# Kernel tuning notes

Measured on AMD Instinct MI355X. Metric: run time of the kernel, lower is better.

Reference implementation:

```python
import jax, jax.numpy as jnp
import numpy as np

N_HEAD = 16
HEAD_DIM = 32          # n_embed // n_head // 2
LAMBDA_INIT = 0.2      # 0.8 - 0.6*exp(-0.3*(layer-1)) with layer=1
ROPE_BASE = 10000.0
EPS = 1e-5


def _rope(x):
    # torchtune RotaryPositionalEmbeddings: interleaved adjacent pairs
    B, T, H, D = x.shape
    half = D // 2
    theta = ROPE_BASE ** (-(jnp.arange(half, dtype=jnp.float32) * 2.0 / D))  # [half]
    ang = jnp.arange(T, dtype=jnp.float32)[:, None] * theta[None, :]         # [T, half]
    cos = jnp.cos(ang)[None, :, None, :]
    sin = jnp.sin(ang)[None, :, None, :]
    xr = x.reshape(B, T, H, half, 2)
    x1, x2 = xr[..., 0], xr[..., 1]
    out = jnp.stack([x1 * cos - x2 * sin, x1 * sin + x2 * cos], axis=-1)
    return out.reshape(B, T, H, D).astype(x.dtype)


def reference(x, W_attn, W_proj, lambda_q1, lambda_k1, lambda_q2, lambda_k2):
    B, T, C = x.shape
    H, D = N_HEAD, HEAD_DIM
    qkv = x @ W_attn                              # [B,T,3C]
    q, k, v = jnp.split(qkv, 3, axis=-1)
    q = _rope(q.reshape(B, T, 2 * H, D)).transpose(0, 2, 1, 3)   # [B,2H,T,D]
    k = _rope(k.reshape(B, T, 2 * H, D)).transpose(0, 2, 1, 3)   # [B,2H,T,D]
    v = v.reshape(B, T, H, 2 * D).transpose(0, 2, 1, 3)          # [B,H,T,2D]

    lam = (jnp.exp(jnp.dot(lambda_q1, lambda_k1))
           - jnp.exp(jnp.dot(lambda_q2, lambda_k2)) + LAMBDA_INIT)

    # causal SDPA over both score paths (2H heads) in one pass, shared V
    scale = 1.0 / jnp.sqrt(jnp.asarray(D, x.dtype))
    scores = jnp.einsum('bhqd,bhkd->bhqk', q, k) * scale         # [B,2H,T,T]
    causal = jnp.tril(jnp.ones((T, T), dtype=bool))
    scores = jnp.where(causal, scores, jnp.finfo(scores.dtype).min)
    probs = jax.nn.softmax(scores, axis=-1)
    vv = jnp.concatenate([v, v], axis=1)                         # [B,2H,T,2D]
    A = jnp.einsum('bhqk,bhkd->bhqd', probs, vv)                 # [B,2H,T,2D]
    A1, A2 = A[:, :H], A[:, H:]

    diff = A1 - lam * A2                                         # [B,H,T,2D]
    # RMSNorm over last dim (2*head_dim), no affine, eps=1e-5
    diff = diff * jax.lax.rsqrt(jnp.mean(diff * diff, axis=-1, keepdims=True) + EPS)
    diff = (1.0 - LAMBDA_INIT) * diff
    out = diff.transpose(0, 2, 1, 3).reshape(B, T, C)
    return out @ W_proj


def setup_inputs() -> dict:
    key = jax.random.key(0)
    ks = jax.random.split(key, 7)
    B, T, C, D = 2, 2048, 1024, HEAD_DIM
    return {
        'x': jax.random.normal(ks[0], (B, T, C), jnp.float32),
        'W_attn': jax.random.normal(ks[1], (C, 3 * C), jnp.float32) * 0.02,
        'W_proj': jax.random.normal(ks[2], (C, C), jnp.float32) * 0.02,
        'lambda_q1': jax.random.normal(ks[3], (D,), jnp.float32) * 0.1,
        'lambda_k1': jax.random.normal(ks[4], (D,), jnp.float32) * 0.1,
        'lambda_q2': jax.random.normal(ks[5], (D,), jnp.float32) * 0.1,
        'lambda_k2': jax.random.normal(ks[6], (D,), jnp.float32) * 0.1,
    }
```

## Files before the change

### kernel.cpp

```cpp
#include <hip/hip_runtime.h>


typedef unsigned short u16;
typedef __bf16 bf16x8 __attribute__((ext_vector_type(8)));
typedef float f32x4 __attribute__((ext_vector_type(4)));
typedef float f32x16 __attribute__((ext_vector_type(16)));
typedef unsigned u32x2 __attribute__((ext_vector_type(2)));

__device__ __forceinline__ u16 f2bf(float f) {
  return __builtin_bit_cast(u16, (__bf16)f);
}
__device__ __forceinline__ float bf2f(u16 u) {
  return (float)__builtin_bit_cast(__bf16, u);
}
__device__ __forceinline__ unsigned pk2(float a, float b) {
  return (unsigned)f2bf(a) | ((unsigned)f2bf(b) << 16);
}

__device__ __forceinline__ void gload16(const u16* g, u16* l) {
  __builtin_amdgcn_global_load_lds(
      (const __attribute__((address_space(1))) unsigned int*)g,
      (__attribute__((address_space(3))) unsigned int*)l, 16, 0, 0);
}

__device__ __forceinline__ void trans_body(const float* __restrict__ in,
                                           u16* __restrict__ out, int R, int Cn,
                                           int bx, int by, float (*tile)[33],
                                           int tx, int ty) {
  const int c0 = bx * 32, r0 = by * 32;
#pragma unroll
  for (int rr = 0; rr < 4; ++rr)
    tile[ty + rr * 8][tx] = in[(size_t)(r0 + ty + rr * 8) * Cn + c0 + tx];
  __syncthreads();
#pragma unroll
  for (int rr = 0; rr < 4; ++rr)
    out[(size_t)(c0 + ty + rr * 8) * R + r0 + tx] = f2bf(tile[tx][ty + rr * 8]);
}

__global__ __launch_bounds__(256) void prep_kernel(
    const float* __restrict__ x, const float* __restrict__ Wa,
    const float* __restrict__ Wp, u16* __restrict__ xb, u16* __restrict__ WaT,
    u16* __restrict__ WpT) {
  __shared__ float tile[32][33];
  const int id = blockIdx.x;
  const int tx = threadIdx.x & 31, ty = threadIdx.x >> 5;
  if (id < 4096) {
    const int i = id * 256 + threadIdx.x;
    float4 v = ((const float4*)x)[i];
    ushort4 o;
    o.x = f2bf(v.x); o.y = f2bf(v.y); o.z = f2bf(v.z); o.w = f2bf(v.w);
    ((ushort4*)xb)[i] = o;
  } else if (id < 7168) {
    const int t = id - 4096;
    trans_body(Wa, WaT, 1024, 3072, t % 96, t / 96, tile, tx, ty);
  } else {
    const int t = id - 7168;
    trans_body(Wp, WpT, 1024, 1024, t & 31, t >> 5, tile, tx, ty);
  }
}

__global__ __launch_bounds__(256) void gemm_bf16_kernel(
    const u16* __restrict__ A, const u16* __restrict__ BT, u16* __restrict__ Cout,
    int Mdim, int Ndim, int Kdim) {
  __shared__ u16 As[128 * 32];
  __shared__ u16 Bs[128 * 32];
  const int tid = threadIdx.x;
  const int l = tid & 63;
  const int w = tid >> 6;
  const int nwgx = gridDim.x;
  const int lin = blockIdx.x + nwgx * blockIdx.y;
  const int cpx = (nwgx * gridDim.y) >> 3;
  const int swz = (lin & 7) * cpx + (lin >> 3);
  const int bm = swz / nwgx, bn = swz % nwgx;
  const int wm = w >> 1, wn = w & 1;
  const int rowA0 = bm * 128, rowB0 = bn * 128;
  const int r_ = tid >> 2;
  const int s_ = (tid & 3) * 8;
  const u16* Ag = &A[(size_t)(rowA0 + r_) * Kdim + s_];
  const u16* Bg = &BT[(size_t)(rowB0 + r_) * Kdim + s_];
  const size_t rstride = (size_t)64 * Kdim;
  f32x4 acc[4][4] = {};
  for (int k0 = 0; k0 < Kdim; k0 += 32) {
    gload16(Ag + k0, &As[r_ * 32 + s_]);
    gload16(Ag + rstride + k0, &As[2048 + r_ * 32 + s_]);
    gload16(Bg + k0, &Bs[r_ * 32 + s_]);
    gload16(Bg + rstride + k0, &Bs[2048 + r_ * 32 + s_]);
    __syncthreads();
    bf16x8 a[4], b[4];
#pragma unroll
    for (int i = 0; i < 4; ++i)
      a[i] = *(const bf16x8*)&As[(wm * 64 + i * 16 + (l & 15)) * 32 + (l >> 4) * 8];
#pragma unroll
    for (int j = 0; j < 4; ++j)
      b[j] = *(const bf16x8*)&Bs[(wn * 64 + j * 16 + (l & 15)) * 32 + (l >> 4) * 8];
#pragma unroll
    for (int i = 0; i < 4; ++i)
#pragma unroll
      for (int j = 0; j < 4; ++j)
        acc[i][j] = __builtin_amdgcn_mfma_f32_16x16x32_bf16(a[i], b[j], acc[i][j], 0, 0, 0);
    __syncthreads();
  }
  const int cr = (l >> 4) * 4;
  const int cc = l & 15;
#pragma unroll
  for (int i = 0; i < 4; ++i)
#pragma unroll
    for (int j = 0; j < 4; ++j)
#pragma unroll
      for (int r = 0; r < 4; ++r) {
        const int row = rowA0 + wm * 64 + i * 16 + cr + r;
        const int col = rowB0 + wn * 64 + j * 16 + cc;
        Cout[(size_t)row * Ndim + col] = f2bf(acc[i][j][r]);
      }
}

__global__ __launch_bounds__(256) void gemm_out_kernel(
    const u16* __restrict__ A, const u16* __restrict__ BT, float* __restrict__ Cout,
    int Mdim, int Ndim, int Kdim) {
  __shared__ u16 As[64 * 32];
  __shared__ u16 Bs[128 * 32];
  const int tid = threadIdx.x;
  const int l = tid & 63;
  const int w = tid >> 6;
  const int nwgx = gridDim.x;
  const int lin = blockIdx.x + nwgx * blockIdx.y;
  const int cpx = (nwgx * gridDim.y) >> 3;
  const int swz = (lin & 7) * cpx + (lin >> 3);
  const int bm = swz / nwgx, bn = swz % nwgx;
  const int wm = w >> 1, wn = w & 1;
  const int rowA0 = bm * 64, rowB0 = bn * 128;
  const int r_ = tid >> 2;
  const int s_ = (tid & 3) * 8;
  const u16* Ag = &A[(size_t)(rowA0 + r_) * Kdim + s_];
  const u16* Bg = &BT[(size_t)(rowB0 + r_) * Kdim + s_];
  const size_t rstride = (size_t)64 * Kdim;
  f32x4 acc[2][4] = {};
  for (int k0 = 0; k0 < Kdim; k0 += 32) {
    gload16(Ag + k0, &As[r_ * 32 + s_]);
    gload16(Bg + k0, &Bs[r_ * 32 + s_]);
    gload16(Bg + rstride + k0, &Bs[2048 + r_ * 32 + s_]);
    __syncthreads();
    bf16x8 a[2], b[4];
#pragma unroll
    for (int i = 0; i < 2; ++i)
      a[i] = *(const bf16x8*)&As[(wm * 32 + i * 16 + (l & 15)) * 32 + (l >> 4) * 8];
#pragma unroll
    for (int j = 0; j < 4; ++j)
      b[j] = *(const bf16x8*)&Bs[(wn * 64 + j * 16 + (l & 15)) * 32 + (l >> 4) * 8];
#pragma unroll
    for (int i = 0; i < 2; ++i)
#pragma unroll
      for (int j = 0; j < 4; ++j)
        acc[i][j] = __builtin_amdgcn_mfma_f32_16x16x32_bf16(a[i], b[j], acc[i][j], 0, 0, 0);
    __syncthreads();
  }
  const int cr = (l >> 4) * 4;
  const int cc = l & 15;
#pragma unroll
  for (int i = 0; i < 2; ++i)
#pragma unroll
    for (int j = 0; j < 4; ++j)
#pragma unroll
      for (int r = 0; r < 4; ++r) {
        const int row = rowA0 + wm * 32 + i * 16 + cr + r;
        const int col = rowB0 + wn * 64 + j * 16 + cc;
        Cout[(size_t)row * Ndim + col] = acc[i][j][r];
      }
}

__global__ __launch_bounds__(256) void rope_vtrans_kernel(
    const u16* __restrict__ qkv, u16* __restrict__ Q, u16* __restrict__ K,
    u16* __restrict__ VT) {
  __shared__ u16 tile[32][33];
  const int id = blockIdx.x;
  const int tid = threadIdx.x;
  if (id < 4096) {
    const int row = id;
    const int b = row >> 11, t = row & 2047;
    const int isK = tid >> 7, hh = (tid >> 2) & 31, i4 = tid & 3;
    const float qsc = isK ? 1.0f : (0.17677669529663687f * 1.4426950408889634f);
    union { uint4 v; u16 s[8]; } in_, out_;
    in_.v = *(const uint4*)&qkv[(size_t)row * 3072 + isK * 1024 + hh * 32 + i4 * 8];
#pragma unroll
    for (int jj = 0; jj < 4; ++jj) {
      const int i = i4 * 4 + jj;
      const float x1 = bf2f(in_.s[2 * jj]), x2 = bf2f(in_.s[2 * jj + 1]);
      const float theta = exp2f(-0.83048202372184059f * (float)i);
      float sn, cs;
      sincosf((float)t * theta, &sn, &cs);
      out_.s[2 * jj] = f2bf((x1 * cs - x2 * sn) * qsc);
      out_.s[2 * jj + 1] = f2bf((x1 * sn + x2 * cs) * qsc);
    }
    u16* dst = isK ? K : Q;
    *(uint4*)&dst[((size_t)(b * 32 + hh) * 2048 + t) * 32 + i4 * 8] = out_.v;
  } else {
    const int id2 = id - 4096;
    const int tx = tid & 31, ty = tid >> 5;
    const int t0 = (id2 & 63) * 32, d0 = ((id2 >> 6) & 1) * 32, bh = id2 >> 7;
    const int b = bh >> 4, hv = bh & 15;
#pragma unroll
    for (int k = 0; k < 4; ++k)
      tile[ty + 8 * k][tx] =
          qkv[(size_t)(b * 2048 + t0 + ty + 8 * k) * 3072 + 2048 + hv * 64 + d0 + tx];
    __syncthreads();
#pragma unroll
    for (int k = 0; k < 4; ++k)
      VT[((size_t)bh * 64 + d0 + ty + 8 * k) * 2048 + t0 + tx] = tile[tx][ty + 8 * k];
  }
}

__global__ __launch_bounds__(256, 4) void attn_kernel(const u16* __restrict__ Q,
                                                      const u16* __restrict__ K,
                                                      const u16* __restrict__ VT,
                                                      u16* __restrict__ PO0,
                                                      u16* __restrict__ PO1,
                                                      float* __restrict__ ML) {
  __shared__ u16 Ks[64 * 34];
  __shared__ u16 Vs[64 * 66];
  __shared__ u16 Os[4 * 32 * 66];
  const int tid = threadIdx.x, l = tid & 63, w = tid >> 6;
  const int pp = blockIdx.x & 7, hf = blockIdx.x >> 3;
  const int h = blockIdx.y, b = blockIdx.z;
  const size_t qkbase = (size_t)(b * 32 + h) * 2048;
  const size_t vtb = (size_t)(b * 16 + (h & 15)) * 64;
  const int lq = l & 31, hi = l >> 5;
  const f32x16 z16 = {};
  const int krow = tid >> 2, ksl = (tid & 3) * 8;
  const int dva = tid >> 3, vsl = (tid & 7) * 8;
  const int dvb = dva + 32;
  const __bf16 one1 = (__bf16)1.0f;
  const bf16x8 ones = {one1, one1, one1, one1, one1, one1, one1, one1};

  for (int halfidx = 0; halfidx < 2; ++halfidx) {
    const int qt = halfidx ? (15 - pp) : pp;
    const int slot = hf ^ halfidx;
    const int s_begin = slot ? (qt + 1) : 0;
    const int s_end = slot ? (2 * qt + 2) : (qt + 1);
    const int q0 = qt * 128;
    const int qw = q0 + w * 32;
    const int q = qw + lq;
    const bf16x8 qf0 = *(const bf16x8*)&Q[(qkbase + q) * 32 + hi * 8];
    const bf16x8 qf1 = *(const bf16x8*)&Q[(qkbase + q) * 32 + 16 + hi * 8];
    f32x16 olo = {}, ohi = {}, lacc = {};
    const u16* pK = &K[(qkbase + s_begin * 64 + krow) * 32 + ksl];
    const u16* pV0 = &VT[(vtb + dva) * 2048 + s_begin * 64 + vsl];
    const u16* pV1 = &VT[(vtb + dvb) * 2048 + s_begin * 64 + vsl];
    uint4 kreg = *(const uint4*)pK;
    uint4 vreg0 = *(const uint4*)pV0;
    uint4 vreg1 = *(const uint4*)pV1;
    for (int s = s_begin; s < s_end; ++s) {
      const int kb = s * 64;
      *(uint4*)&Ks[krow * 34 + ksl] = kreg;
      *(uint4*)&Vs[dva * 66 + vsl] = vreg0;
      *(uint4*)&Vs[dvb * 66 + vsl] = vreg1;
      const int adv = (s + 1 < s_end) ? 1 : 0;
      pK += adv * 2048;
      pV0 += adv * 64;
      pV1 += adv * 64;
      kreg = *(const uint4*)pK;
      vreg0 = *(const uint4*)pV0;
      vreg1 = *(const uint4*)pV1;
      __syncthreads();
      if (qw + 31 >= kb) {
        f32x16 s0_, s1_;
        {
          const bf16x8 ka0 = *(const bf16x8*)&Ks[lq * 34 + hi * 8];
          const bf16x8 ka1 = *(const bf16x8*)&Ks[lq * 34 + 16 + hi * 8];
          const bf16x8 kc0 = *(const bf16x8*)&Ks[(32 + lq) * 34 + hi * 8];
          const bf16x8 kc1 = *(const bf16x8*)&Ks[(32 + lq) * 34 + 16 + hi * 8];
          __builtin_amdgcn_s_setprio(1);
          s0_ = __builtin_amdgcn_mfma_f32_32x32x16_bf16(ka0, qf0, z16, 0, 0, 0);
          s0_ = __builtin_amdgcn_mfma_f32_32x32x16_bf16(ka1, qf1, s0_, 0, 0, 0);
          s1_ = __builtin_amdgcn_mfma_f32_32x32x16_bf16(kc0, qf0, z16, 0, 0, 0);
          s1_ = __builtin_amdgcn_mfma_f32_32x32x16_bf16(kc1, qf1, s1_, 0, 0, 0);
          __builtin_amdgcn_s_setprio(0);
        }
        const bool nm = (kb + 63 > qw);
        if (nm) {
#pragma unroll
          for (int r = 0; r < 16; ++r) {
            const int kr = (r & 3) + 8 * (r >> 2) + 4 * hi;
            if (kb + kr > q) s0_[r] = -1e30f;
            if (kb + 32 + kr > q) s1_[r] = -1e30f;
          }
        }
#pragma unroll
        for (int r = 0; r < 16; ++r) {
          s0_[r] = __builtin_amdgcn_exp2f(s0_[r]);
          s1_[r] = __builtin_amdgcn_exp2f(s1_[r]);
        }
        unsigned pw[16];
#pragma unroll
        for (int j = 0; j < 8; ++j) {
          pw[j] = pk2(s0_[2 * j], s0_[2 * j + 1]);
          pw[8 + j] = pk2(s1_[2 * j], s1_[2 * j + 1]);
        }
        bf16x8 pa[4];
#pragma unroll
        for (int fidx = 0; fidx < 4; ++fidx) {
          const unsigned* wt = &pw[fidx * 4];
          union { unsigned u[4]; bf16x8 v; } fr;
#if __has_builtin(__builtin_amdgcn_permlane32_swap)
          const u32x2 rA = __builtin_amdgcn_permlane32_swap(wt[0], wt[2], false, false);
          const u32x2 rB = __builtin_amdgcn_permlane32_swap(wt[1], wt[3], false, false);
          fr.u[0] = rA[0]; fr.u[1] = rB[0]; fr.u[2] = rA[1]; fr.u[3] = rB[1];
#else
          const unsigned ua = hi ? wt[0] : wt[2];
          const unsigned ub = hi ? wt[1] : wt[3];
          const unsigned sa = __shfl_xor(ua, 32, 64);
          const unsigned sb = __shfl_xor(ub, 32, 64);
          fr.u[0] = hi ? sa : wt[0];
          fr.u[1] = hi ? sb : wt[1];
          fr.u[2] = hi ? wt[2] : sa;
          fr.u[3] = hi ? wt[3] : sb;
#endif
          pa[fidx] = fr.v;
        }
        __builtin_amdgcn_s_setprio(1);
#pragma unroll
        for (int ks = 0; ks < 4; ++ks) {
          const bf16x8 va = *(const bf16x8*)&Vs[lq * 66 + ks * 16 + hi * 8];
          const bf16x8 vb = *(const bf16x8*)&Vs[(32 + lq) * 66 + ks * 16 + hi * 8];
          olo = __builtin_amdgcn_mfma_f32_32x32x16_bf16(va, pa[ks], olo, 0, 0, 0);
          ohi = __builtin_amdgcn_mfma_f32_32x32x16_bf16(vb, pa[ks], ohi, 0, 0, 0);
          lacc = __builtin_amdgcn_mfma_f32_32x32x16_bf16(ones, pa[ks], lacc, 0, 0, 0);
        }
        __builtin_amdgcn_s_setprio(0);
      }
      __syncthreads();
    }
    const float lsum = lacc[0];
    const float inv = (lsum > 0.f) ? (1.0f / lsum) : 0.f;
    if (hi == 0)
      ML[(size_t)slot * 131072 + qkbase + q] = lsum;
    u16* Ow = &Os[(w * 32 + lq) * 66];
#pragma unroll
    for (int g = 0; g < 4; ++g) {
      const int d0 = 8 * g + 4 * hi;
      *(unsigned*)&Ow[d0] = pk2(olo[4 * g] * inv, olo[4 * g + 1] * inv);
      *(unsigned*)&Ow[d0 + 2] = pk2(olo[4 * g + 2] * inv, olo[4 * g + 3] * inv);
      *(unsigned*)&Ow[32 + d0] = pk2(ohi[4 * g] * inv, ohi[4 * g + 1] * inv);
      *(unsigned*)&Ow[32 + d0 + 2] = pk2(ohi[4 * g + 2] * inv, ohi[4 * g + 3] * inv);
    }
    __syncthreads();
    u16* PO = slot ? PO1 : PO0;
    for (int s2 = tid; s2 < 1024; s2 += 256) {
      const int wv = s2 >> 8, qq = (s2 >> 3) & 31, sl = (s2 & 7) * 8;
      *(uint4*)&PO[(qkbase + q0 + wv * 32 + qq) * 64 + sl] =
          *(const uint4*)&Os[(wv * 32 + qq) * 66 + sl];
    }
    __syncthreads();
  }
}

__global__ __launch_bounds__(256) void diff_rms_kernel(
    const u16* __restrict__ PO0, const u16* __restrict__ PO1,
    const float* __restrict__ ML,
    const float* __restrict__ lq1, const float* __restrict__ lk1,
    const float* __restrict__ lq2, const float* __restrict__ lk2,
    u16* __restrict__ Mb) {
  const int g = threadIdx.x >> 5;
  const int dl = (threadIdx.x & 31) * 2;
  const int ridx = blockIdx.x * 8 + g;
  const int b = ridx >> 15, rem = ridx & 32767, h = rem >> 11, t = rem & 2047;
  float d1 = 0.f, d2 = 0.f;
#pragma unroll
  for (int i = 0; i < 32; ++i) {
    d1 += lq1[i] * lk1[i];
    d2 += lq2[i] * lk2[i];
  }
  const float lam = expf(d1) - expf(d2) + 0.2f;
  const size_t row1 = (size_t)(b * 32 + h) * 2048 + t;
  const size_t row2 = (size_t)(b * 32 + 16 + h) * 2048 + t;
  const float lA1 = ML[row1], lB1 = ML[131072 + row1];
  const float lA2 = ML[row2], lB2 = ML[131072 + row2];
  const float i1 = 1.0f / (lA1 + lB1);
  const float wa1 = lA1 * i1, wb1 = lB1 * i1;
  const float i2 = 1.0f / (lA2 + lB2);
  const float wa2 = lA2 * i2, wb2 = lB2 * i2;
  const ushort2 p01 = *(const ushort2*)&PO0[row1 * 64 + dl];
  const ushort2 p11 = *(const ushort2*)&PO1[row1 * 64 + dl];
  const ushort2 p02 = *(const ushort2*)&PO0[row2 * 64 + dl];
  const ushort2 p12 = *(const ushort2*)&PO1[row2 * 64 + dl];
  const float a1x = wa1 * bf2f(p01.x) + wb1 * bf2f(p11.x);
  const float a1y = wa1 * bf2f(p01.y) + wb1 * bf2f(p11.y);
  const float a2x = wa2 * bf2f(p02.x) + wb2 * bf2f(p12.x);
  const float a2y = wa2 * bf2f(p02.y) + wb2 * bf2f(p12.y);
  const float df0 = a1x - lam * a2x;
  const float df1 = a1y - lam * a2y;
  float ss = df0 * df0 + df1 * df1;
  ss += __shfl_xor(ss, 1, 64);
  ss += __shfl_xor(ss, 2, 64);
  ss += __shfl_xor(ss, 4, 64);
  ss += __shfl_xor(ss, 8, 64);
  ss += __shfl_xor(ss, 16, 64);
  const float rms = rsqrtf(ss * (1.0f / 64.0f) + 1e-5f);
  ushort2 o;
  o.x = f2bf(0.8f * df0 * rms);
  o.y = f2bf(0.8f * df1 * rms);
  *(ushort2*)&Mb[((size_t)(b * 2048 + t)) * 1024 + h * 64 + dl] = o;
}

extern "C" void kernel_launch(void* const* d_in, const int* in_sizes, int n_in,
                              void* d_out, int out_size, void* d_ws, size_t ws_size,
                              hipStream_t stream) {
  const float* x = (const float*)d_in[0];
  const float* Wa = (const float*)d_in[1];
  const float* Wp = (const float*)d_in[2];
  const float* lq1 = (const float*)d_in[3];
  const float* lk1 = (const float*)d_in[4];
  const float* lq2 = (const float*)d_in[5];
  const float* lk2 = (const float*)d_in[6];
  if (ws_size < (size_t)(64u << 20)) return;

  char* ws = (char*)d_ws;
  u16* Qarr = (u16*)(ws);
  u16* Karr = (u16*)(ws + (8u << 20));
  u16* VTarr = (u16*)(ws + (16u << 20));
  u16* WpT = (u16*)(ws + (24u << 20));
  char* arena = ws + (26u << 20);
  u16* xb = (u16*)(arena);
  u16* WaT = (u16*)(arena + (8u << 20));
  u16* qkvb = (u16*)(arena + (14u << 20));
  u16* PO0 = (u16*)(arena);
  u16* PO1 = (u16*)(arena + (16u << 20));
  float* ML = (float*)(arena + (32u << 20));
  u16* Mbuf = Qarr;

  prep_kernel<<<8192, 256, 0, stream>>>(x, Wa, Wp, xb, WaT, WpT);
  gemm_bf16_kernel<<<dim3(24, 32), 256, 0, stream>>>(xb, WaT, qkvb, 4096, 3072, 1024);
  rope_vtrans_kernel<<<8192, 256, 0, stream>>>(qkvb, Qarr, Karr, VTarr);
  attn_kernel<<<dim3(16, 32, 2), 256, 0, stream>>>(Qarr, Karr, VTarr, PO0, PO1, ML);
  diff_rms_kernel<<<8192, 256, 0, stream>>>(PO0, PO1, ML, lq1, lk1, lq2, lk2, Mbuf);
  gemm_out_kernel<<<dim3(8, 64), 256, 0, stream>>>(Mbuf, WpT, (float*)d_out, 4096, 1024, 1024);
}
```

Measured before the change: 145.8 us.

## Fuse RoPE and V transpose into QKV GEMM epilogue, precompute rope table and lambda

```diff
diff --git a/kernel.cpp b/kernel.cpp
--- a/kernel.cpp
+++ b/kernel.cpp
@@ -39,8 +39,10 @@
 
 __global__ __launch_bounds__(256) void prep_kernel(
     const float* __restrict__ x, const float* __restrict__ Wa,
-    const float* __restrict__ Wp, u16* __restrict__ xb, u16* __restrict__ WaT,
-    u16* __restrict__ WpT) {
+    const float* __restrict__ Wp, const float* __restrict__ lq1,
+    const float* __restrict__ lk1, const float* __restrict__ lq2,
+    const float* __restrict__ lk2, u16* __restrict__ xb, u16* __restrict__ WaT,
+    u16* __restrict__ WpT, float2* __restrict__ Tab, float* __restrict__ lamp) {
   __shared__ float tile[32][33];
   const int id = blockIdx.x;
   const int tx = threadIdx.x & 31, ty = threadIdx.x >> 5;
@@ -53,15 +55,32 @@
   } else if (id < 7168) {
     const int t = id - 4096;
     trans_body(Wa, WaT, 1024, 3072, t % 96, t / 96, tile, tx, ty);
-  } else {
+  } else if (id < 8192) {
     const int t = id - 7168;
     trans_body(Wp, WpT, 1024, 1024, t & 31, t >> 5, tile, tx, ty);
+  } else if (id < 8320) {
+    const int idx = (id - 8192) * 256 + threadIdx.x;
+    const int t = idx >> 4, i = idx & 15;
+    const float theta = exp2f(-0.83048202372184059f * (float)i);
+    float sn, cs;
+    sincosf((float)t * theta, &sn, &cs);
+    Tab[idx] = make_float2(cs, sn);
+  } else if (threadIdx.x == 0) {
+    float d1 = 0.f, d2 = 0.f;
+#pragma unroll
+    for (int i = 0; i < 32; ++i) {
+      d1 += lq1[i] * lk1[i];
+      d2 += lq2[i] * lk2[i];
+    }
+    *lamp = expf(d1) - expf(d2) + 0.2f;
   }
 }
 
-__global__ __launch_bounds__(256) void gemm_bf16_kernel(
-    const u16* __restrict__ A, const u16* __restrict__ BT, u16* __restrict__ Cout,
-    int Mdim, int Ndim, int Kdim) {
+__global__ __launch_bounds__(256) void gemm_qkv_kernel(
+    const u16* __restrict__ A, const u16* __restrict__ BT,
+    u16* __restrict__ Q, u16* __restrict__ K, u16* __restrict__ VT,
+    const float2* __restrict__ Tab) {
+  const int Kdim = 1024;
   __shared__ u16 As[128 * 32];
   __shared__ u16 Bs[128 * 32];
   const int tid = threadIdx.x;
@@ -102,16 +121,49 @@
   }
   const int cr = (l >> 4) * 4;
   const int cc = l & 15;
-#pragma unroll
-  for (int i = 0; i < 4; ++i)
-#pragma unroll
-    for (int j = 0; j < 4; ++j)
-#pragma unroll
-      for (int r = 0; r < 4; ++r) {
-        const int row = rowA0 + wm * 64 + i * 16 + cr + r;
-        const int col = rowB0 + wn * 64 + j * 16 + cc;
-        Cout[(size_t)row * Ndim + col] = f2bf(acc[i][j][r]);
+  const int region = bn >> 3;
+  if (region < 2) {
+    const float qsc_ = (region == 0) ? 0.25503486f : 1.0f;
+    u16* dst = (region == 0) ? Q : K;
+#pragma unroll
+    for (int i = 0; i < 4; ++i) {
+      const int row0 = rowA0 + wm * 64 + i * 16 + cr;
+      const int b_ = row0 >> 11, t0 = row0 & 2047;
+#pragma unroll
+      for (int j = 0; j < 4; ++j) {
+        const int c = (bn & 7) * 128 + wn * 64 + j * 16 + cc;
+        const int hh = c >> 5, d = c & 31;
+        const int ii = d >> 1;
+        const float sgn = (d & 1) ? 1.0f : -1.0f;
+        const size_t base = (size_t)(b_ * 32 + hh) * 2048;
+#pragma unroll
+        for (int r = 0; r < 4; ++r) {
+          const int t = t0 + r;
+          const float2 cs = Tab[t * 16 + ii];
+          const float xv = acc[i][j][r];
+          const float px = __shfl_xor(xv, 1, 64);
+          dst[(base + t) * 32 + d] = f2bf((xv * cs.x + sgn * px * cs.y) * qsc_);
+        }
       }
+    }
+  } else {
+#pragma unroll
+    for (int i = 0; i < 4; ++i) {
+      const int row0 = rowA0 + wm * 64 + i * 16 + cr;
+      const int b_ = row0 >> 11, t0 = row0 & 2047;
+#pragma unroll
+      for (int j = 0; j < 4; ++j) {
+        const int c3 = (bn & 7) * 128 + wn * 64 + j * 16 + cc;
+        const int hv = c3 >> 6, dv = c3 & 63;
+        ushort4 ov;
+        ov.x = f2bf(acc[i][j][0]);
+        ov.y = f2bf(acc[i][j][1]);
+        ov.z = f2bf(acc[i][j][2]);
+        ov.w = f2bf(acc[i][j][3]);
+        *(ushort4*)&VT[((size_t)(b_ * 16 + hv) * 64 + dv) * 2048 + t0] = ov;
+      }
+    }
+  }
 }
 
 __global__ __launch_bounds__(256) void gemm_out_kernel(
@@ -166,47 +218,6 @@
         const int col = rowB0 + wn * 64 + j * 16 + cc;
         Cout[(size_t)row * Ndim + col] = acc[i][j][r];
       }
-}
-
-__global__ __launch_bounds__(256) void rope_vtrans_kernel(
-    const u16* __restrict__ qkv, u16* __restrict__ Q, u16* __restrict__ K,
-    u16* __restrict__ VT) {
-  __shared__ u16 tile[32][33];
-  const int id = blockIdx.x;
-  const int tid = threadIdx.x;
-  if (id < 4096) {
-    const int row = id;
-    const int b = row >> 11, t = row & 2047;
-    const int isK = tid >> 7, hh = (tid >> 2) & 31, i4 = tid & 3;
-    const float qsc = isK ? 1.0f : (0.17677669529663687f * 1.4426950408889634f);
-    union { uint4 v; u16 s[8]; } in_, out_;
-    in_.v = *(const uint4*)&qkv[(size_t)row * 3072 + isK * 1024 + hh * 32 + i4 * 8];
-#pragma unroll
-    for (int jj = 0; jj < 4; ++jj) {
-      const int i = i4 * 4 + jj;
-      const float x1 = bf2f(in_.s[2 * jj]), x2 = bf2f(in_.s[2 * jj + 1]);
-      const float theta = exp2f(-0.83048202372184059f * (float)i);
-      float sn, cs;
-      sincosf((float)t * theta, &sn, &cs);
-      out_.s[2 * jj] = f2bf((x1 * cs - x2 * sn) * qsc);
-      out_.s[2 * jj + 1] = f2bf((x1 * sn + x2 * cs) * qsc);
-    }
-    u16* dst = isK ? K : Q;
-    *(uint4*)&dst[((size_t)(b * 32 + hh) * 2048 + t) * 32 + i4 * 8] = out_.v;
-  } else {
-    const int id2 = id - 4096;
-    const int tx = tid & 31, ty = tid >> 5;
-    const int t0 = (id2 & 63) * 32, d0 = ((id2 >> 6) & 1) * 32, bh = id2 >> 7;
-    const int b = bh >> 4, hv = bh & 15;
-#pragma unroll
-    for (int k = 0; k < 4; ++k)
-      tile[ty + 8 * k][tx] =
-          qkv[(size_t)(b * 2048 + t0 + ty + 8 * k) * 3072 + 2048 + hv * 64 + d0 + tx];
-    __syncthreads();
-#pragma unroll
-    for (int k = 0; k < 4; ++k)
-      VT[((size_t)bh * 64 + d0 + ty + 8 * k) * 2048 + t0 + tx] = tile[tx][ty + 8 * k];
-  }
 }
 
 __global__ __launch_bounds__(256, 4) void attn_kernel(const u16* __restrict__ Q,
@@ -355,21 +366,13 @@
 
 __global__ __launch_bounds__(256) void diff_rms_kernel(
     const u16* __restrict__ PO0, const u16* __restrict__ PO1,
-    const float* __restrict__ ML,
-    const float* __restrict__ lq1, const float* __restrict__ lk1,
-    const float* __restrict__ lq2, const float* __restrict__ lk2,
+    const float* __restrict__ ML, const float* __restrict__ lamp,
     u16* __restrict__ Mb) {
   const int g = threadIdx.x >> 5;
   const int dl = (threadIdx.x & 31) * 2;
   const int ridx = blockIdx.x * 8 + g;
   const int b = ridx >> 15, rem = ridx & 32767, h = rem >> 11, t = rem & 2047;
-  float d1 = 0.f, d2 = 0.f;
-#pragma unroll
-  for (int i = 0; i < 32; ++i) {
-    d1 += lq1[i] * lk1[i];
-    d2 += lq2[i] * lk2[i];
-  }
-  const float lam = expf(d1) - expf(d2) + 0.2f;
+  const float lam = *lamp;
   const size_t row1 = (size_t)(b * 32 + h) * 2048 + t;
   const size_t row2 = (size_t)(b * 32 + 16 + h) * 2048 + t;
   const float lA1 = ML[row1], lB1 = ML[131072 + row1];
@@ -421,16 +424,17 @@
   char* arena = ws + (26u << 20);
   u16* xb = (u16*)(arena);
   u16* WaT = (u16*)(arena + (8u << 20));
-  u16* qkvb = (u16*)(arena + (14u << 20));
+  float2* Tab = (float2*)(arena + (14u << 20));
   u16* PO0 = (u16*)(arena);
   u16* PO1 = (u16*)(arena + (16u << 20));
   float* ML = (float*)(arena + (32u << 20));
+  float* lamp = (float*)(arena + (33u << 20));
   u16* Mbuf = Qarr;
 
-  prep_kernel<<<8192, 256, 0, stream>>>(x, Wa, Wp, xb, WaT, WpT);
-  gemm_bf16_kernel<<<dim3(24, 32), 256, 0, stream>>>(xb, WaT, qkvb, 4096, 3072, 1024);
-  rope_vtrans_kernel<<<8192, 256, 0, stream>>>(qkvb, Qarr, Karr, VTarr);
+  prep_kernel<<<8321, 256, 0, stream>>>(x, Wa, Wp, lq1, lk1, lq2, lk2,
+                                        xb, WaT, WpT, Tab, lamp);
+  gemm_qkv_kernel<<<dim3(24, 32), 256, 0, stream>>>(xb, WaT, Qarr, Karr, VTarr, Tab);
   attn_kernel<<<dim3(16, 32, 2), 256, 0, stream>>>(Qarr, Karr, VTarr, PO0, PO1, ML);
-  diff_rms_kernel<<<8192, 256, 0, stream>>>(PO0, PO1, ML, lq1, lk1, lq2, lk2, Mbuf);
+  diff_rms_kernel<<<8192, 256, 0, stream>>>(PO0, PO1, ML, lamp, Mbuf);
   gemm_out_kernel<<<dim3(8, 64), 256, 0, stream>>>(Mbuf, WpT, (float*)d_out, 4096, 1024, 1024);
 }
```

New measurement: 142.6 us. 1.02x faster.
